# Kernel tuning notes

Measured on AMD Instinct MI355X. Metric: run time of the kernel, lower is better.

Reference implementation:

```python
import jax, jax.numpy as jnp
import numpy as np
import math

HIDDEN = 2048
NUM_HEADS = 16
HEAD_DIM = HIDDEN // NUM_HEADS  # 128
B, T = 2, 2048
MAX_POS = 4096
ROPE_BASE = 10000.0


def _rope_cache(dim, max_pos, base):
    inv_freq = 1.0 / (base ** (jnp.arange(0, dim, 2, dtype=jnp.float32) / dim))
    t = jnp.arange(max_pos, dtype=jnp.float32)
    freqs = jnp.einsum('i,j->ij', t, inv_freq)        # [max_pos, dim/2]
    emb = jnp.concatenate([freqs, freqs], axis=-1)     # [max_pos, dim]
    return jnp.cos(emb), jnp.sin(emb)


def setup_inputs() -> dict:
    key = jax.random.key(0)
    ks = jax.random.split(key, 5)
    hidden_states = jax.random.normal(ks[0], (B, T, HIDDEN), dtype=jnp.float32)
    # additive causal mask, large negative (not -inf) for numerical safety
    causal = jnp.triu(jnp.full((T, T), -1e9, dtype=jnp.float32), k=1)
    attention_mask = causal[None, None, :, :]          # [1,1,T,T]
    position_ids = jnp.arange(T, dtype=jnp.int64)
    s = 1.0 / math.sqrt(HIDDEN)
    Wq = jax.random.normal(ks[1], (HIDDEN, HIDDEN), dtype=jnp.float32) * s
    Wk = jax.random.normal(ks[2], (HIDDEN, HIDDEN), dtype=jnp.float32) * s
    Wv = jax.random.normal(ks[3], (HIDDEN, HIDDEN), dtype=jnp.float32) * s
    Wo = jax.random.normal(ks[4], (HIDDEN, HIDDEN), dtype=jnp.float32) * s
    cos_cached, sin_cached = _rope_cache(HEAD_DIM, MAX_POS, ROPE_BASE)
    return {
        'hidden_states': hidden_states,
        'attention_mask': attention_mask,
        'position_ids': position_ids,
        'Wq': Wq, 'Wk': Wk, 'Wv': Wv, 'Wo': Wo,
        'cos_cached': cos_cached, 'sin_cached': sin_cached,
    }


def _apply_rope(x, cos, sin):
    # x: [B, T, nh, hd]; cos/sin: [T, 1, hd] (broadcast over heads)
    x1 = x[..., 0::2]
    x2 = x[..., 1::2]
    x_rot = jnp.stack([-x2, x1], axis=-1).reshape(x.shape)  # interleaved rotate
    return x * cos + x_rot * sin


def reference(hidden_states, attention_mask, position_ids, Wq, Wk, Wv, Wo,
              cos_cached, sin_cached):
    Bs, Ts, H = hidden_states.shape
    nh, hd = NUM_HEADS, HEAD_DIM
    q = (hidden_states @ Wq.T).reshape(Bs, Ts, nh, hd)
    k = (hidden_states @ Wk.T).reshape(Bs, Ts, nh, hd)
    v = (hidden_states @ Wv.T).reshape(Bs, Ts, nh, hd)
    cos = cos_cached[position_ids][:, None, :]  # [T,1,hd]
    sin = sin_cached[position_ids][:, None, :]
    q = _apply_rope(q, cos, sin)
    k = _apply_rope(k, cos, sin)
    # [B, nh, T, hd]
    q = q.transpose(0, 2, 1, 3)
    k = k.transpose(0, 2, 1, 3)
    v = v.transpose(0, 2, 1, 3)
    scores = jnp.einsum('bhqd,bhkd->bhqk', q, k) / math.sqrt(hd)
    scores = scores + attention_mask
    attn = jax.nn.softmax(scores, axis=-1)
    out = jnp.einsum('bhqk,bhkd->bhqd', attn, v)
    out = out.transpose(0, 2, 1, 3).reshape(Bs, Ts, H)
    return out @ Wo.T
```

## Files before the change

kernel.cpp:

```cpp
#include <hip/hip_runtime.h>
#include <cstdint>


typedef __bf16 v8bf __attribute__((ext_vector_type(8)));
typedef float  v4f  __attribute__((ext_vector_type(4)));
typedef float  f32x16 __attribute__((ext_vector_type(16)));

__device__ __forceinline__ uint16_t f2bf(float f) {
  union { float f; uint32_t u; } v; v.f = f;
  uint32_t u = v.u;
  return (uint16_t)((u + 0x7FFFu + ((u >> 16) & 1u)) >> 16);
}

__device__ __forceinline__ uint32_t cvtpk(float lo, float hi) {
  uint32_t w;
  asm("v_cvt_pk_bf16_f32 %0, %1, %2" : "=v"(w) : "v"(lo), "v"(hi));
  return w;
}

__device__ __forceinline__ void gload16(const void* g, void* l) {
  __builtin_amdgcn_global_load_lds(
      (const __attribute__((address_space(1))) void*)g,
      (__attribute__((address_space(3))) void*)l, 16, 0, 0);
}

__global__ void cvt_all_kernel(const float* __restrict__ s0, uint16_t* d0,
                               const float* __restrict__ s1, uint16_t* d1,
                               const float* __restrict__ s2, uint16_t* d2,
                               const float* __restrict__ s3, uint16_t* d3,
                               const float* __restrict__ s4, uint16_t* d4) {
  const float* src; uint16_t* dst; int n4;
  switch (blockIdx.y) {
    case 0: src = s0; dst = d0; n4 = 2097152; break;
    case 1: src = s1; dst = d1; n4 = 1048576; break;
    case 2: src = s2; dst = d2; n4 = 1048576; break;
    case 3: src = s3; dst = d3; n4 = 1048576; break;
    default: src = s4; dst = d4; n4 = 1048576; break;
  }
  int i = blockIdx.x * blockDim.x + threadIdx.x;
  int stride = gridDim.x * blockDim.x;
  for (; i < n4; i += stride) {
    float4 v = reinterpret_cast<const float4*>(src)[i];
    ushort4 o;
    o.x = f2bf(v.x); o.y = f2bf(v.y); o.z = f2bf(v.z); o.w = f2bf(v.w);
    reinterpret_cast<ushort4*>(dst)[i] = o;
  }
}

__device__ __forceinline__ void gemm256_mainloop(
    const uint16_t* __restrict__ A, const uint16_t* __restrict__ Bt,
    int m0, int n0, uint16_t* As, uint16_t* Bs, v4f acc[4][4]) {
  const int tid  = threadIdx.x;
  const int lane = tid & 63, w = tid >> 6;
  const int wm = w >> 1, wn = w & 1;
  const int lrow = lane & 15, lhi = lane >> 4;

  auto stageA = [&](int buf, int k0, int i) {
    int c = i * 512 + tid;
    int row = c >> 3, seg = c & 7;
    int sseg = seg ^ (row & 7);
    gload16(A + (size_t)(m0 + row) * 2048 + k0 + sseg * 8,
            As + buf * 16384 + c * 8);
  };
  auto stageB = [&](int buf, int k0, int i) {
    int c = i * 512 + tid;
    int row = c >> 3, seg = c & 7;
    int sseg = seg ^ (row & 7);
    gload16(Bt + (size_t)(n0 + row) * 2048 + k0 + sseg * 8,
            Bs + buf * 8192 + c * 8);
  };

#pragma unroll
  for (int i = 0; i < 4; ++i) stageA(0, 0, i);
#pragma unroll
  for (int i = 0; i < 2; ++i) stageB(0, 0, i);
#pragma unroll
  for (int i = 0; i < 4; ++i) stageA(1, 64, i);
#pragma unroll
  for (int i = 0; i < 2; ++i) stageB(1, 64, i);
  asm volatile("s_waitcnt vmcnt(6)" ::: "memory");
  __builtin_amdgcn_s_barrier();
  __builtin_amdgcn_sched_barrier(0);

  for (int t = 0; t < 32; ++t) {
    const int cb = t % 3;
    const int sb = (t + 2) % 3;
    const int sk = (t + 2) * 64;
    const uint16_t* Ac = As + cb * 16384;
    const uint16_t* Bc = Bs + cb * 8192;
    const bool ds = (t + 2) < 32;

    v8bf af[2][4], bfv[2][4];
#pragma unroll
    for (int mf = 0; mf < 4; ++mf) {
      const int ar = wm * 64 + mf * 16 + lrow;
      af[0][mf] = *reinterpret_cast<const v8bf*>(
          Ac + ar * 64 + ((lhi ^ (ar & 7)) * 8));
    }
#pragma unroll
    for (int nf = 0; nf < 4; ++nf) {
      const int br = wn * 64 + nf * 16 + lrow;
      bfv[0][nf] = *reinterpret_cast<const v8bf*>(
          Bc + br * 64 + ((lhi ^ (br & 7)) * 8));
    }
    if (ds) { stageA(sb, sk, 0); stageA(sb, sk, 1); stageB(sb, sk, 0); }
#pragma unroll
    for (int mf = 0; mf < 4; ++mf) {
      const int ar = wm * 64 + mf * 16 + lrow;
      af[1][mf] = *reinterpret_cast<const v8bf*>(
          Ac + ar * 64 + (((4 + lhi) ^ (ar & 7)) * 8));
    }
#pragma unroll
    for (int nf = 0; nf < 4; ++nf) {
      const int br = wn * 64 + nf * 16 + lrow;
      bfv[1][nf] = *reinterpret_cast<const v8bf*>(
          Bc + br * 64 + (((4 + lhi) ^ (br & 7)) * 8));
    }
    if (ds) { stageA(sb, sk, 2); stageA(sb, sk, 3); stageB(sb, sk, 1); }

    if (t < 30) asm volatile("s_waitcnt vmcnt(6)" ::: "memory");
    else        asm volatile("s_waitcnt vmcnt(0)" ::: "memory");
    __builtin_amdgcn_s_barrier();
    __builtin_amdgcn_sched_barrier(0);
    __builtin_amdgcn_s_setprio(1);
#pragma unroll
    for (int ks = 0; ks < 2; ++ks)
#pragma unroll
      for (int mf = 0; mf < 4; ++mf)
#pragma unroll
        for (int nf = 0; nf < 4; ++nf)
          acc[mf][nf] = __builtin_amdgcn_mfma_f32_16x16x32_bf16(
              af[ks][mf], bfv[ks][nf], acc[mf][nf], 0, 0, 0);
    __builtin_amdgcn_s_setprio(0);
    asm volatile("" ::: "memory");
    __builtin_amdgcn_s_barrier();
    __builtin_amdgcn_sched_barrier(0);
  }
}

__global__ __launch_bounds__(512, 2) void qkv_gemm_kernel(
    const uint16_t* __restrict__ Xbf,
    const uint16_t* __restrict__ Wqb, const uint16_t* __restrict__ Wkb,
    const uint16_t* __restrict__ Wvb,
    const float* __restrict__ cosc, const float* __restrict__ sinc,
    uint16_t* __restrict__ Qh, uint16_t* __restrict__ Kh,
    uint16_t* __restrict__ Vt) {
  __shared__ uint16_t As[3 * 256 * 64];
  __shared__ uint16_t Bs[3 * 128 * 64];
  const int id  = blockIdx.x;
  const int swz = (id & 7) * 96 + (id >> 3);
  const int which = swz >> 8;
  const int rem = swz & 255;
  const int m0 = (rem >> 4) * 256, n0 = (rem & 15) * 128;
  const uint16_t* Wb = (which == 0) ? Wqb : (which == 1) ? Wkb : Wvb;

  v4f acc[4][4];
#pragma unroll
  for (int i = 0; i < 4; ++i)
#pragma unroll
    for (int j = 0; j < 4; ++j) acc[i][j] = (v4f)0.0f;

  gemm256_mainloop(Xbf, Wb, m0, n0, As, Bs, acc);

  const int lane = threadIdx.x & 63;
  const int w = threadIdx.x >> 6, wm = w >> 1, wn = w & 1;
  const int lrow = lane & 15, lhi = lane >> 4;
  const int b = m0 >> 11;

  if (which < 2) {
    uint16_t* dst = (which == 0) ? Qh : Kh;
#pragma unroll
    for (int mf = 0; mf < 4; ++mf) {
#pragma unroll
      for (int nf = 0; nf < 4; ++nf) {
        const int n = n0 + wn * 64 + nf * 16 + lrow;
        const int head = n >> 7, d = n & 127;
#pragma unroll
        for (int r = 0; r < 4; ++r) {
          const int m = m0 + wm * 64 + mf * 16 + lhi * 4 + r;
          const int t = m & 2047;
          float v = acc[mf][nf][r];
          float p = __shfl_xor(v, 1);
          float rot = (n & 1) ? p : -p;
          float cf = cosc[t * 128 + d], sf = sinc[t * 128 + d];
          dst[((size_t)(b * 16 + head) * 2048 + t) * 128 + d] =
              f2bf(v * cf + rot * sf);
        }
      }
    }
  } else {
#pragma unroll
    for (int mf = 0; mf < 4; ++mf) {
#pragma unroll
      for (int nf = 0; nf < 4; ++nf) {
        const int n = n0 + wn * 64 + nf * 16 + lrow;
        const int head = n >> 7, d = n & 127;
        const int m = m0 + wm * 64 + mf * 16 + lhi * 4;
        const int t = m & 2047;
        ushort4 o;
        o.x = f2bf(acc[mf][nf][0]); o.y = f2bf(acc[mf][nf][1]);
        o.z = f2bf(acc[mf][nf][2]); o.w = f2bf(acc[mf][nf][3]);
        *reinterpret_cast<ushort4*>(
            &Vt[((size_t)(b * 16 + head) * 128 + d) * 2048 + t]) = o;
      }
    }
  }
}

__global__ __launch_bounds__(256, 2) void attn_kernel(
    const uint16_t* __restrict__ Qh, const uint16_t* __restrict__ Kh,
    const uint16_t* __restrict__ Vt, uint16_t* __restrict__ Ob) {
  __shared__ uint16_t Ks[2 * 64 * 128];
  __shared__ uint16_t Vs[2 * 128 * 64];

  const int id = blockIdx.x;
  const int qt = (id < 256) ? (15 - (id >> 5)) : ((id - 256) >> 5);
  const int bh = id & 31;
  const int tid = threadIdx.x, lane = tid & 63, w = tid >> 6;
  const int l31 = lane & 31, hi = lane >> 5;
  const size_t base = (size_t)bh * 2048 * 128;
  const int q0 = qt * 128 + w * 32;
  const int qr = q0 + l31;

  v8bf qf[8];
#pragma unroll
  for (int ks = 0; ks < 8; ++ks)
    qf[ks] = *reinterpret_cast<const v8bf*>(
        Qh + base + (size_t)qr * 128 + ks * 16 + hi * 8);

  f32x16 acc[4];
#pragma unroll
  for (int d = 0; d < 4; ++d) acc[d] = (f32x16)0.0f;
  float m = -1e30f, l = 0.0f;

  auto stage = [&](int buf, int kt) {
    uint16_t* Kd = Ks + buf * 8192;
    uint16_t* Vd = Vs + buf * 8192;
#pragma unroll
    for (int i = 0; i < 4; ++i) {
      int c = i * 256 + tid;
      int row = c >> 4, seg = c & 15;
      int sseg = seg ^ (row & 15);
      gload16(Kh + base + (size_t)(kt * 64 + row) * 128 + sseg * 8,
              Kd + c * 8);
    }
#pragma unroll
    for (int i = 0; i < 4; ++i) {
      int c = i * 256 + tid;
      int row = c >> 3, seg = c & 7;
      int sseg = seg ^ (row & 7);
      gload16(Vt + base + (size_t)row * 2048 + kt * 64 + sseg * 8,
              Vd + c * 8);
    }
  };

  const float sc = 0.08838834764831845f;
  const int nkt = 2 * (qt + 1);
  stage(0, 0);
  for (int kt = 0; kt < nkt; ++kt) {
    const int cur = kt & 1;
    asm volatile("s_waitcnt vmcnt(0)" ::: "memory");
    __builtin_amdgcn_s_barrier();
    __builtin_amdgcn_sched_barrier(0);
    if (kt + 1 < nkt) stage(cur ^ 1, kt + 1);
    const uint16_t* Kc = Ks + cur * 8192;
    const uint16_t* Vc = Vs + cur * 8192;

    if (kt * 64 <= q0 + 31) {
      f32x16 s[2];
      s[0] = (f32x16)0.0f; s[1] = (f32x16)0.0f;
#pragma unroll
      for (int kb = 0; kb < 2; ++kb) {
        const int row = kb * 32 + l31;
        const int swzk = row & 15;
#pragma unroll
        for (int ks = 0; ks < 8; ++ks) {
          const int seg = (ks * 2 + hi) ^ swzk;
          v8bf kf = *reinterpret_cast<const v8bf*>(Kc + row * 128 + seg * 8);
          s[kb] = __builtin_amdgcn_mfma_f32_32x32x16_bf16(kf, qf[ks], s[kb],
                                                          0, 0, 0);
        }
      }
      if (kt * 64 + 63 > q0) {
#pragma unroll
        for (int kb = 0; kb < 2; ++kb)
#pragma unroll
          for (int q = 0; q < 4; ++q)
#pragma unroll
            for (int r = 0; r < 4; ++r) {
              const int kc = kt * 64 + kb * 32 + q * 8 + hi * 4 + r;
              float v = s[kb][q * 4 + r] * sc;
              s[kb][q * 4 + r] = (kc > qr) ? -1e30f : v;
            }
      } else {
#pragma unroll
        for (int kb = 0; kb < 2; ++kb)
#pragma unroll
          for (int g = 0; g < 16; ++g) s[kb][g] *= sc;
      }
      float t8[8];
#pragma unroll
      for (int g = 0; g < 8; ++g)
        t8[g] = fmaxf(fmaxf(s[0][g], s[0][g + 8]),
                      fmaxf(s[1][g], s[1][g + 8]));
      float mx = fmaxf(fmaxf(fmaxf(t8[0], t8[1]), fmaxf(t8[2], t8[3])),
                       fmaxf(fmaxf(t8[4], t8[5]), fmaxf(t8[6], t8[7])));
      mx = fmaxf(mx, __shfl_xor(mx, 32));
      if (!__all(mx - m <= 8.0f)) {
        const float mnew = fmaxf(m, mx);
        const float so = __expf(m - mnew);
        m = mnew;
        l *= so;
#pragma unroll
        for (int d = 0; d < 4; ++d)
#pragma unroll
          for (int g = 0; g < 16; ++g) acc[d][g] *= so;
      }
      float rs = 0.0f;
#pragma unroll
      for (int kb = 0; kb < 2; ++kb)
#pragma unroll
        for (int g = 0; g < 16; ++g) {
          const float pv = __expf(s[kb][g] - m);
          s[kb][g] = pv;
          rs += pv;
        }
      rs += __shfl_xor(rs, 32);
      l += rs;
      union BW { uint32_t w[4]; v8bf v; };
      BW pb[4];
#pragma unroll
      for (int kb = 0; kb < 2; ++kb)
#pragma unroll
        for (int sl = 0; sl < 2; ++sl) {
          uint32_t a0 = cvtpk(s[kb][8 * sl + 0], s[kb][8 * sl + 1]);
          uint32_t a1 = cvtpk(s[kb][8 * sl + 2], s[kb][8 * sl + 3]);
          uint32_t b0 = cvtpk(s[kb][8 * sl + 4], s[kb][8 * sl + 5]);
          uint32_t b1 = cvtpk(s[kb][8 * sl + 6], s[kb][8 * sl + 7]);
          asm("v_permlane32_swap_b32 %0, %1" : "+v"(a0), "+v"(b0));
          asm("v_permlane32_swap_b32 %0, %1" : "+v"(a1), "+v"(b1));
          BW& f = pb[kb * 2 + sl];
          f.w[0] = a0; f.w[1] = a1; f.w[2] = b0; f.w[3] = b1;
        }
#pragma unroll
      for (int d = 0; d < 4; ++d) {
        const int row = d * 32 + l31;
        const int swzv = row & 7;
#pragma unroll
        for (int sl4 = 0; sl4 < 4; ++sl4) {
          const int seg = (sl4 * 2 + hi) ^ swzv;
          v8bf va = *reinterpret_cast<const v8bf*>(Vc + row * 64 + seg * 8);
          acc[d] = __builtin_amdgcn_mfma_f32_32x32x16_bf16(va, pb[sl4].v,
                                                           acc[d], 0, 0, 0);
        }
      }
    }
  }

  asm volatile("s_waitcnt vmcnt(0) lgkmcnt(0)" ::: "memory");
  __builtin_amdgcn_s_barrier();
  __builtin_amdgcn_sched_barrier(0);
  uint32_t* L32 = reinterpret_cast<uint32_t*>(&Ks[0]);
  const float inv = 1.0f / l;
#pragma unroll
  for (int d = 0; d < 4; ++d)
#pragma unroll
    for (int q = 0; q < 4; ++q)
#pragma unroll
      for (int rp = 0; rp < 2; ++rp) {
        const int dd1 = d * 16 + q * 4 + hi * 2 + rp;
        const uint32_t lo16 = f2bf(acc[d][q * 4 + rp * 2] * inv);
        const uint32_t hi16 = f2bf(acc[d][q * 4 + rp * 2 + 1] * inv);
        L32[(w * 32 + l31) * 64 + (dd1 ^ ((l31 & 7) << 3))] =
            lo16 | (hi16 << 16);
      }
  asm volatile("" ::: "memory");
  __builtin_amdgcn_s_barrier();
  __builtin_amdgcn_sched_barrier(0);
  const int b = bh >> 4, head = bh & 15;
  uint32_t* Og = reinterpret_cast<uint32_t*>(Ob);
#pragma unroll
  for (int j = 0; j < 32; ++j) {
    const int qrow = qt * 128 + w * 32 + j;
    const uint32_t v = L32[(w * 32 + j) * 64 + (lane ^ ((j & 7) << 3))];
    Og[((size_t)(b * 2048 + qrow) * 2048 + head * 128) / 2 + lane] = v;
  }
}

__global__ __launch_bounds__(512, 2) void out_gemm_kernel(
    const uint16_t* __restrict__ Abf, const uint16_t* __restrict__ Wob,
    float* __restrict__ out) {
  __shared__ uint16_t As[3 * 256 * 64];
  __shared__ uint16_t Bs[3 * 128 * 64];
  const int id  = blockIdx.x;
  const int swz = (id & 7) * 32 + (id >> 3);
  const int m0 = (swz >> 4) * 256, n0 = (swz & 15) * 128;
  v4f acc[4][4];
#pragma unroll
  for (int i = 0; i < 4; ++i)
#pragma unroll
    for (int j = 0; j < 4; ++j) acc[i][j] = (v4f)0.0f;

  gemm256_mainloop(Abf, Wob, m0, n0, As, Bs, acc);

  const int lane = threadIdx.x & 63;
  const int w = threadIdx.x >> 6, wm = w >> 1, wn = w & 1;
  const int lrow = lane & 15, lhi = lane >> 4;
#pragma unroll
  for (int mf = 0; mf < 4; ++mf)
#pragma unroll
    for (int nf = 0; nf < 4; ++nf) {
      const int n = n0 + wn * 64 + nf * 16 + lrow;
#pragma unroll
      for (int r = 0; r < 4; ++r) {
        const int m = m0 + wm * 64 + mf * 16 + lhi * 4 + r;
        out[(size_t)m * 2048 + n] = acc[mf][nf][r];
      }
    }
}

extern "C" void kernel_launch(void* const* d_in, const int* in_sizes, int n_in,
                              void* d_out, int out_size, void* d_ws,
                              size_t ws_size, hipStream_t stream) {
  const float* hidden = (const float*)d_in[0];
  const float* Wq = (const float*)d_in[3];
  const float* Wk = (const float*)d_in[4];
  const float* Wv = (const float*)d_in[5];
  const float* Wo = (const float*)d_in[6];
  const float* cosc = (const float*)d_in[7];
  const float* sinc = (const float*)d_in[8];
  float* out = (float*)d_out;

  uint16_t* Wqb = (uint16_t*)d_ws;
  uint16_t* Wkb = Wqb + 4194304;
  uint16_t* Wvb = Wkb + 4194304;
  uint16_t* Wob = Wvb + 4194304;
  uint16_t* Xbf = Wob + 4194304;
  uint16_t* Qh  = Xbf + 8388608;
  uint16_t* Kh  = Qh + 8388608;
  uint16_t* Vt  = Kh + 8388608;
  uint16_t* Ob  = Xbf;

  cvt_all_kernel<<<dim3(512, 5), 256, 0, stream>>>(
      hidden, Xbf, Wq, Wqb, Wk, Wkb, Wv, Wvb, Wo, Wob);

  qkv_gemm_kernel<<<dim3(768), 512, 0, stream>>>(
      Xbf, Wqb, Wkb, Wvb, cosc, sinc, Qh, Kh, Vt);

  attn_kernel<<<dim3(512), 256, 0, stream>>>(Qh, Kh, Vt, Ob);

  out_gemm_kernel<<<dim3(256), 512, 0, stream>>>(Ob, Wob, out);
}
```

Baseline: 394.3 us.

## Use 256x256 tiles with a 10-slot rotating LDS ring in QKV GEMM

```diff
diff --git a/kernel.cpp b/kernel.cpp
--- a/kernel.cpp
+++ b/kernel.cpp
@@ -47,7 +47,206 @@
   }
 }
 
-__device__ __forceinline__ void gemm256_mainloop(
+__device__ __forceinline__ int wrap10(int x) { return x >= 10 ? x - 10 : x; }
+
+__global__ __launch_bounds__(512, 1) void qkv_gemm_kernel(
+    const uint16_t* __restrict__ Xbf,
+    const uint16_t* __restrict__ Wqb, const uint16_t* __restrict__ Wkb,
+    const uint16_t* __restrict__ Wvb,
+    const float* __restrict__ cosc, const float* __restrict__ sinc,
+    uint16_t* __restrict__ Qh, uint16_t* __restrict__ Kh,
+    uint16_t* __restrict__ Vt) {
+  __shared__ uint16_t L[10 * 8192];
+  const int id  = blockIdx.x;
+  const int swz = (id & 7) * 48 + (id >> 3);
+  const int which = swz >> 7;
+  const int rem = swz & 127;
+  const int m0 = (rem >> 3) * 256, n0 = (rem & 7) * 256;
+  const uint16_t* Wb = (which == 0) ? Wqb : (which == 1) ? Wkb : Wvb;
+
+  const int tid = threadIdx.x, lane = tid & 63, w = tid >> 6;
+  const int wm = w >> 2, wn = w & 3;
+  const int lrow = lane & 15, lhi = lane >> 4;
+  const int brl = (wn & 1) * 64;
+
+  v4f acc[8][4];
+#pragma unroll
+  for (int i = 0; i < 8; ++i)
+#pragma unroll
+    for (int j = 0; j < 4; ++j) acc[i][j] = (v4f)0.0f;
+
+  auto stage_part = [&](const uint16_t* S, int rbase, int slot, int k0) {
+#pragma unroll
+    for (int i = 0; i < 2; ++i) {
+      int c = i * 512 + tid;
+      int row = c >> 3, seg = c & 7;
+      int sseg = seg ^ (row & 7);
+      gload16(S + (size_t)(rbase + row) * 2048 + k0 + sseg * 8,
+              L + slot * 8192 + c * 8);
+    }
+  };
+
+  stage_part(Xbf, m0, 0, 0);
+  stage_part(Xbf, m0 + 128, 1, 0);
+  stage_part(Wb, n0, 2, 0);
+  stage_part(Wb, n0 + 128, 3, 0);
+  stage_part(Xbf, m0, 4, 64);
+  stage_part(Xbf, m0 + 128, 5, 64);
+  asm volatile("s_waitcnt vmcnt(4)" ::: "memory");
+  __builtin_amdgcn_s_barrier();
+  __builtin_amdgcn_sched_barrier(0);
+
+  int sbase = 0;
+  for (int t = 0; t < 32; ++t) {
+    const uint16_t* Aw = L + wrap10(sbase + wm) * 8192;
+    const uint16_t* Bw = L + wrap10(sbase + 2 + (wn >> 1)) * 8192;
+    const int kt1 = (t + 1) * 64, kt2 = (t + 2) * 64;
+    const bool st1 = (t + 1) < 32, st2 = (t + 2) < 32;
+    v8bf af[4], bf[4];
+
+#pragma unroll
+    for (int f = 0; f < 4; ++f) {
+      const int lr = f * 16 + lrow;
+      af[f] = *reinterpret_cast<const v8bf*>(
+          Aw + lr * 64 + ((lhi ^ (lr & 7)) * 8));
+    }
+#pragma unroll
+    for (int f = 0; f < 4; ++f) {
+      const int lr = brl + f * 16 + lrow;
+      bf[f] = *reinterpret_cast<const v8bf*>(
+          Bw + lr * 64 + ((lhi ^ (lr & 7)) * 8));
+    }
+    if (st1) stage_part(Wb, n0, wrap10(sbase + 6), kt1);
+    __builtin_amdgcn_s_barrier();
+    asm volatile("s_waitcnt lgkmcnt(0)" ::: "memory");
+    __builtin_amdgcn_sched_barrier(0);
+    __builtin_amdgcn_s_setprio(1);
+#pragma unroll
+    for (int mf = 0; mf < 4; ++mf)
+#pragma unroll
+      for (int nf = 0; nf < 4; ++nf)
+        acc[mf][nf] = __builtin_amdgcn_mfma_f32_16x16x32_bf16(
+            af[mf], bf[nf], acc[mf][nf], 0, 0, 0);
+    __builtin_amdgcn_s_setprio(0);
+    __builtin_amdgcn_s_barrier();
+    __builtin_amdgcn_sched_barrier(0);
+
+#pragma unroll
+    for (int f = 0; f < 4; ++f) {
+      const int lr = 64 + f * 16 + lrow;
+      af[f] = *reinterpret_cast<const v8bf*>(
+          Aw + lr * 64 + ((lhi ^ (lr & 7)) * 8));
+    }
+    if (st1) stage_part(Wb, n0 + 128, wrap10(sbase + 7), kt1);
+    __builtin_amdgcn_s_barrier();
+    asm volatile("s_waitcnt lgkmcnt(0)" ::: "memory");
+    __builtin_amdgcn_sched_barrier(0);
+    __builtin_amdgcn_s_setprio(1);
+#pragma unroll
+    for (int mf = 0; mf < 4; ++mf)
+#pragma unroll
+      for (int nf = 0; nf < 4; ++nf)
+        acc[4 + mf][nf] = __builtin_amdgcn_mfma_f32_16x16x32_bf16(
+            af[mf], bf[nf], acc[4 + mf][nf], 0, 0, 0);
+    __builtin_amdgcn_s_setprio(0);
+    __builtin_amdgcn_s_barrier();
+    __builtin_amdgcn_sched_barrier(0);
+
+#pragma unroll
+    for (int f = 0; f < 4; ++f) {
+      const int lr = f * 16 + lrow;
+      af[f] = *reinterpret_cast<const v8bf*>(
+          Aw + lr * 64 + (((4 + lhi) ^ (lr & 7)) * 8));
+    }
+#pragma unroll
+    for (int f = 0; f < 4; ++f) {
+      const int lr = brl + f * 16 + lrow;
+      bf[f] = *reinterpret_cast<const v8bf*>(
+          Bw + lr * 64 + (((4 + lhi) ^ (lr & 7)) * 8));
+    }
+    if (st2) stage_part(Xbf, m0, wrap10(sbase + 8), kt2);
+    __builtin_amdgcn_s_barrier();
+    asm volatile("s_waitcnt lgkmcnt(0)" ::: "memory");
+    __builtin_amdgcn_sched_barrier(0);
+    __builtin_amdgcn_s_setprio(1);
+#pragma unroll
+    for (int mf = 0; mf < 4; ++mf)
+#pragma unroll
+      for (int nf = 0; nf < 4; ++nf)
+        acc[mf][nf] = __builtin_amdgcn_mfma_f32_16x16x32_bf16(
+            af[mf], bf[nf], acc[mf][nf], 0, 0, 0);
+    __builtin_amdgcn_s_setprio(0);
+    __builtin_amdgcn_s_barrier();
+    __builtin_amdgcn_sched_barrier(0);
+
+#pragma unroll
+    for (int f = 0; f < 4; ++f) {
+      const int lr = 64 + f * 16 + lrow;
+      af[f] = *reinterpret_cast<const v8bf*>(
+          Aw + lr * 64 + (((4 + lhi) ^ (lr & 7)) * 8));
+    }
+    if (st2) stage_part(Xbf, m0 + 128, wrap10(sbase + 9), kt2);
+    __builtin_amdgcn_s_barrier();
+    asm volatile("s_waitcnt lgkmcnt(0)" ::: "memory");
+    __builtin_amdgcn_sched_barrier(0);
+    __builtin_amdgcn_s_setprio(1);
+#pragma unroll
+    for (int mf = 0; mf < 4; ++mf)
+#pragma unroll
+      for (int nf = 0; nf < 4; ++nf)
+        acc[4 + mf][nf] = __builtin_amdgcn_mfma_f32_16x16x32_bf16(
+            af[mf], bf[nf], acc[4 + mf][nf], 0, 0, 0);
+    __builtin_amdgcn_s_setprio(0);
+    if (t < 30) asm volatile("s_waitcnt vmcnt(4)" ::: "memory");
+    else        asm volatile("s_waitcnt vmcnt(0)" ::: "memory");
+    __builtin_amdgcn_s_barrier();
+    __builtin_amdgcn_sched_barrier(0);
+
+    sbase = wrap10(sbase + 4);
+  }
+
+  const int b = m0 >> 11;
+  if (which < 2) {
+    uint16_t* dst = (which == 0) ? Qh : Kh;
+#pragma unroll
+    for (int mf = 0; mf < 8; ++mf) {
+#pragma unroll
+      for (int nf = 0; nf < 4; ++nf) {
+        const int n = n0 + wn * 64 + nf * 16 + lrow;
+        const int head = n >> 7, d = n & 127;
+#pragma unroll
+        for (int r = 0; r < 4; ++r) {
+          const int m = m0 + wm * 128 + mf * 16 + lhi * 4 + r;
+          const int tt = m & 2047;
+          float v = acc[mf][nf][r];
+          float p = __shfl_xor(v, 1);
+          float rot = (n & 1) ? p : -p;
+          float cf = cosc[tt * 128 + d], sf = sinc[tt * 128 + d];
+          dst[((size_t)(b * 16 + head) * 2048 + tt) * 128 + d] =
+              f2bf(v * cf + rot * sf);
+        }
+      }
+    }
+  } else {
+#pragma unroll
+    for (int mf = 0; mf < 8; ++mf) {
+#pragma unroll
+      for (int nf = 0; nf < 4; ++nf) {
+        const int n = n0 + wn * 64 + nf * 16 + lrow;
+        const int head = n >> 7, d = n & 127;
+        const int m = m0 + wm * 128 + mf * 16 + lhi * 4;
+        const int tt = m & 2047;
+        ushort4 o;
+        o.x = f2bf(acc[mf][nf][0]); o.y = f2bf(acc[mf][nf][1]);
+        o.z = f2bf(acc[mf][nf][2]); o.w = f2bf(acc[mf][nf][3]);
+        *reinterpret_cast<ushort4*>(
+            &Vt[((size_t)(b * 16 + head) * 128 + d) * 2048 + tt]) = o;
+      }
+    }
+  }
+}
+
+__device__ __forceinline__ void gemm256x128_mainloop(
     const uint16_t* __restrict__ A, const uint16_t* __restrict__ Bt,
     int m0, int n0, uint16_t* As, uint16_t* Bs, v4f acc[4][4]) {
   const int tid  = threadIdx.x;
@@ -88,123 +287,79 @@
     const int sk = (t + 2) * 64;
     const uint16_t* Ac = As + cb * 16384;
     const uint16_t* Bc = Bs + cb * 8192;
-    const bool ds = (t + 2) < 32;
-
-    v8bf af[2][4], bfv[2][4];
-#pragma unroll
-    for (int mf = 0; mf < 4; ++mf) {
-      const int ar = wm * 64 + mf * 16 + lrow;
-      af[0][mf] = *reinterpret_cast<const v8bf*>(
-          Ac + ar * 64 + ((lhi ^ (ar & 7)) * 8));
-    }
-#pragma unroll
-    for (int nf = 0; nf < 4; ++nf) {
-      const int br = wn * 64 + nf * 16 + lrow;
-      bfv[0][nf] = *reinterpret_cast<const v8bf*>(
-          Bc + br * 64 + ((lhi ^ (br & 7)) * 8));
-    }
-    if (ds) { stageA(sb, sk, 0); stageA(sb, sk, 1); stageB(sb, sk, 0); }
-#pragma unroll
-    for (int mf = 0; mf < 4; ++mf) {
-      const int ar = wm * 64 + mf * 16 + lrow;
-      af[1][mf] = *reinterpret_cast<const v8bf*>(
-          Ac + ar * 64 + (((4 + lhi) ^ (ar & 7)) * 8));
-    }
-#pragma unroll
-    for (int nf = 0; nf < 4; ++nf) {
-      const int br = wn * 64 + nf * 16 + lrow;
-      bfv[1][nf] = *reinterpret_cast<const v8bf*>(
-          Bc + br * 64 + (((4 + lhi) ^ (br & 7)) * 8));
-    }
-    if (ds) { stageA(sb, sk, 2); stageA(sb, sk, 3); stageB(sb, sk, 1); }
-
-    if (t < 30) asm volatile("s_waitcnt vmcnt(6)" ::: "memory");
-    else        asm volatile("s_waitcnt vmcnt(0)" ::: "memory");
-    __builtin_amdgcn_s_barrier();
-    __builtin_amdgcn_sched_barrier(0);
-    __builtin_amdgcn_s_setprio(1);
-#pragma unroll
-    for (int ks = 0; ks < 2; ++ks)
+    const bool do_stage = (t + 2) < 32;
+#pragma unroll
+    for (int ks = 0; ks < 2; ++ks) {
+      v8bf af[4], bfv[4];
+#pragma unroll
+      for (int mf = 0; mf < 4; ++mf) {
+        const int ar = wm * 64 + mf * 16 + lrow;
+        const int seg = (ks * 4 + lhi) ^ (ar & 7);
+        af[mf] = *reinterpret_cast<const v8bf*>(Ac + ar * 64 + seg * 8);
+      }
+#pragma unroll
+      for (int nf = 0; nf < 4; ++nf) {
+        const int br = wn * 64 + nf * 16 + lrow;
+        const int seg = (ks * 4 + lhi) ^ (br & 7);
+        bfv[nf] = *reinterpret_cast<const v8bf*>(Bc + br * 64 + seg * 8);
+      }
+      if (do_stage) {
+        if (ks == 0) { stageA(sb, sk, 0); stageA(sb, sk, 1); stageB(sb, sk, 0); }
+        else         { stageA(sb, sk, 2); stageA(sb, sk, 3); stageB(sb, sk, 1); }
+      }
+      if (ks == 1) {
+        if (t < 30) asm volatile("s_waitcnt vmcnt(6)" ::: "memory");
+        else        asm volatile("s_waitcnt vmcnt(0)" ::: "memory");
+      } else {
+        asm volatile("" ::: "memory");
+      }
+      __builtin_amdgcn_s_barrier();
+      __builtin_amdgcn_sched_barrier(0);
+      __builtin_amdgcn_s_setprio(1);
 #pragma unroll
       for (int mf = 0; mf < 4; ++mf)
 #pragma unroll
         for (int nf = 0; nf < 4; ++nf)
           acc[mf][nf] = __builtin_amdgcn_mfma_f32_16x16x32_bf16(
-              af[ks][mf], bfv[ks][nf], acc[mf][nf], 0, 0, 0);
-    __builtin_amdgcn_s_setprio(0);
-    asm volatile("" ::: "memory");
-    __builtin_amdgcn_s_barrier();
-    __builtin_amdgcn_sched_barrier(0);
-  }
-}
-
-__global__ __launch_bounds__(512, 2) void qkv_gemm_kernel(
-    const uint16_t* __restrict__ Xbf,
-    const uint16_t* __restrict__ Wqb, const uint16_t* __restrict__ Wkb,
-    const uint16_t* __restrict__ Wvb,
-    const float* __restrict__ cosc, const float* __restrict__ sinc,
-    uint16_t* __restrict__ Qh, uint16_t* __restrict__ Kh,
-    uint16_t* __restrict__ Vt) {
+              af[mf], bfv[nf], acc[mf][nf], 0, 0, 0);
+      __builtin_amdgcn_s_setprio(0);
+      asm volatile("" ::: "memory");
+      __builtin_amdgcn_s_barrier();
+      __builtin_amdgcn_sched_barrier(0);
+    }
+  }
+}
+
+__global__ __launch_bounds__(512, 2) void out_gemm_kernel(
+    const uint16_t* __restrict__ Abf, const uint16_t* __restrict__ Wob,
+    float* __restrict__ out) {
   __shared__ uint16_t As[3 * 256 * 64];
   __shared__ uint16_t Bs[3 * 128 * 64];
   const int id  = blockIdx.x;
-  const int swz = (id & 7) * 96 + (id >> 3);
-  const int which = swz >> 8;
-  const int rem = swz & 255;
-  const int m0 = (rem >> 4) * 256, n0 = (rem & 15) * 128;
-  const uint16_t* Wb = (which == 0) ? Wqb : (which == 1) ? Wkb : Wvb;
-
+  const int swz = (id & 7) * 32 + (id >> 3);
+  const int m0 = (swz >> 4) * 256, n0 = (swz & 15) * 128;
   v4f acc[4][4];
 #pragma unroll
   for (int i = 0; i < 4; ++i)
 #pragma unroll
     for (int j = 0; j < 4; ++j) acc[i][j] = (v4f)0.0f;
 
-  gemm256_mainloop(Xbf, Wb, m0, n0, As, Bs, acc);
+  gemm256x128_mainloop(Abf, Wob, m0, n0, As, Bs, acc);
 
   const int lane = threadIdx.x & 63;
   const int w = threadIdx.x >> 6, wm = w >> 1, wn = w & 1;
   const int lrow = lane & 15, lhi = lane >> 4;
-  const int b = m0 >> 11;
-
-  if (which < 2) {
-    uint16_t* dst = (which == 0) ? Qh : Kh;
-#pragma unroll
-    for (int mf = 0; mf < 4; ++mf) {
-#pragma unroll
-      for (int nf = 0; nf < 4; ++nf) {
-        const int n = n0 + wn * 64 + nf * 16 + lrow;
-        const int head = n >> 7, d = n & 127;
-#pragma unroll
-        for (int r = 0; r < 4; ++r) {
-          const int m = m0 + wm * 64 + mf * 16 + lhi * 4 + r;
-          const int t = m & 2047;
-          float v = acc[mf][nf][r];
-          float p = __shfl_xor(v, 1);
-          float rot = (n & 1) ? p : -p;
-          float cf = cosc[t * 128 + d], sf = sinc[t * 128 + d];
-          dst[((size_t)(b * 16 + head) * 2048 + t) * 128 + d] =
-              f2bf(v * cf + rot * sf);
-        }
-      }
-    }
-  } else {
-#pragma unroll
-    for (int mf = 0; mf < 4; ++mf) {
-#pragma unroll
-      for (int nf = 0; nf < 4; ++nf) {
-        const int n = n0 + wn * 64 + nf * 16 + lrow;
-        const int head = n >> 7, d = n & 127;
-        const int m = m0 + wm * 64 + mf * 16 + lhi * 4;
-        const int t = m & 2047;
-        ushort4 o;
-        o.x = f2bf(acc[mf][nf][0]); o.y = f2bf(acc[mf][nf][1]);
-        o.z = f2bf(acc[mf][nf][2]); o.w = f2bf(acc[mf][nf][3]);
-        *reinterpret_cast<ushort4*>(
-            &Vt[((size_t)(b * 16 + head) * 128 + d) * 2048 + t]) = o;
-      }
-    }
-  }
+#pragma unroll
+  for (int mf = 0; mf < 4; ++mf)
+#pragma unroll
+    for (int nf = 0; nf < 4; ++nf) {
+      const int n = n0 + wn * 64 + nf * 16 + lrow;
+#pragma unroll
+      for (int r = 0; r < 4; ++r) {
+        const int m = m0 + wm * 64 + mf * 16 + lhi * 4 + r;
+        out[(size_t)m * 2048 + n] = acc[mf][nf][r];
+      }
+    }
 }
 
 __global__ __launch_bounds__(256, 2) void attn_kernel(
@@ -387,38 +542,6 @@
   }
 }
 
-__global__ __launch_bounds__(512, 2) void out_gemm_kernel(
-    const uint16_t* __restrict__ Abf, const uint16_t* __restrict__ Wob,
-    float* __restrict__ out) {
-  __shared__ uint16_t As[3 * 256 * 64];
-  __shared__ uint16_t Bs[3 * 128 * 64];
-  const int id  = blockIdx.x;
-  const int swz = (id & 7) * 32 + (id >> 3);
-  const int m0 = (swz >> 4) * 256, n0 = (swz & 15) * 128;
-  v4f acc[4][4];
-#pragma unroll
-  for (int i = 0; i < 4; ++i)
-#pragma unroll
-    for (int j = 0; j < 4; ++j) acc[i][j] = (v4f)0.0f;
-
-  gemm256_mainloop(Abf, Wob, m0, n0, As, Bs, acc);
-
-  const int lane = threadIdx.x & 63;
-  const int w = threadIdx.x >> 6, wm = w >> 1, wn = w & 1;
-  const int lrow = lane & 15, lhi = lane >> 4;
-#pragma unroll
-  for (int mf = 0; mf < 4; ++mf)
-#pragma unroll
-    for (int nf = 0; nf < 4; ++nf) {
-      const int n = n0 + wn * 64 + nf * 16 + lrow;
-#pragma unroll
-      for (int r = 0; r < 4; ++r) {
-        const int m = m0 + wm * 64 + mf * 16 + lhi * 4 + r;
-        out[(size_t)m * 2048 + n] = acc[mf][nf][r];
-      }
-    }
-}
-
 extern "C" void kernel_launch(void* const* d_in, const int* in_sizes, int n_in,
                               void* d_out, int out_size, void* d_ws,
                               size_t ws_size, hipStream_t stream) {
@@ -444,7 +567,7 @@
   cvt_all_kernel<<<dim3(512, 5), 256, 0, stream>>>(
       hidden, Xbf, Wq, Wqb, Wk, Wkb, Wv, Wvb, Wo, Wob);
 
-  qkv_gemm_kernel<<<dim3(768), 512, 0, stream>>>(
+  qkv_gemm_kernel<<<dim3(384), 512, 0, stream>>>(
       Xbf, Wqb, Wkb, Wvb, cosc, sinc, Qh, Kh, Vt);
 
   attn_kernel<<<dim3(512), 256, 0, stream>>>(Qh, Kh, Vt, Ob);
```

Result: faster. 383.2 us (-2.8%).
